# Kernel tuning notes

Hardware: AMD Instinct MI355X
Metric: run time of the kernel (lower is better)

The kernel has to match this reference:

```python
import jax, jax.numpy as jnp
import numpy as np

B, S, D, H = 4, 2048, 768, 12
DH = D // H  # 64
SCALE = float(DH)  # att_scale == 'per_head' -> dim // num_heads


def setup_inputs() -> dict:
    key = jax.random.key(0)
    ks = jax.random.split(key, 7)
    p = 1.0 / np.sqrt(D)
    return {
        "x": jax.random.normal(ks[0], (B, S, D), dtype=jnp.float32),
        "Wq": jax.random.normal(ks[1], (D, D), dtype=jnp.float32) * p,
        "bq": jax.random.normal(ks[2], (D,), dtype=jnp.float32) * p,
        "Wk": jax.random.normal(ks[3], (D, D), dtype=jnp.float32) * p,
        "bk": jax.random.normal(ks[4], (D,), dtype=jnp.float32) * p,
        "Wv": jax.random.normal(ks[5], (D, D), dtype=jnp.float32) * p,
        "bv": jax.random.normal(ks[6], (D,), dtype=jnp.float32) * p,
    }


def reference(x, Wq, bq, Wk, bk, Wv, bv):
    # torch nn.Linear: y = x @ W.T + b
    q = x @ Wq.T + bq  # [B,S,D]
    k = x @ Wk.T + bk
    v = x @ Wv.T + bv
    # split heads -> [B,H,S,DH]
    def heads(t):
        return t.reshape(B, S, H, DH).transpose(0, 2, 1, 3)
    q, k, v = heads(q), heads(k), heads(v)
    scores = jnp.einsum("bhqd,bhkd->bhqk", q, k) / jnp.sqrt(jnp.float32(SCALE))
    probs = jax.nn.softmax(scores, axis=-1)
    h = jnp.einsum("bhqk,bhkd->bhqd", probs, v)  # [B,H,S,DH]
    return h.transpose(0, 2, 1, 3).reshape(B, S, D)
```

## Files before the change

### kernel.cpp

```cpp
#include <hip/hip_runtime.h>

#define NB 4
#define NS 2048
#define ND 768
#define NH 12
#define NDH 64
#define NM (NB * NS)

typedef __attribute__((ext_vector_type(8))) _Float16 f16x8;
typedef __attribute__((ext_vector_type(4))) _Float16 f16x4;
typedef __attribute__((ext_vector_type(2))) _Float16 f16x2;
typedef __attribute__((ext_vector_type(8))) unsigned short u16x8;
typedef __attribute__((ext_vector_type(4))) unsigned short u16x4;
typedef __attribute__((ext_vector_type(4))) float f32x4;

__device__ __forceinline__ unsigned short f2h(float f) {
    _Float16 h = (_Float16)f;
    return __builtin_bit_cast(unsigned short, h);
}
__device__ __forceinline__ f16x8 ldf16x8(const unsigned short* p) {
    return __builtin_bit_cast(f16x8, *(const u16x8*)p);
}
__device__ __forceinline__ f16x4 ldf16x4(const unsigned short* p) {
    return __builtin_bit_cast(f16x4, *(const u16x4*)p);
}
__device__ __forceinline__ void gload_lds16(const void* g, void* l) {
    __builtin_amdgcn_global_load_lds(
        (const __attribute__((address_space(1))) void*)g,
        (__attribute__((address_space(3))) void*)l, 16, 0, 0);
}

__device__ __forceinline__ float exp2_fast(float x) {
#if __has_builtin(__builtin_amdgcn_exp2f)
    return __builtin_amdgcn_exp2f(x);
#else
    return exp2f(x);
#endif
}

__device__ __forceinline__ float max3f(float a, float b, float c) {
    return fmaxf(fmaxf(a, b), c);
}

__device__ __forceinline__ f16x4 pk4(float a, float b, float c, float d) {
#if __has_builtin(__builtin_amdgcn_cvt_pkrtz)
    f16x2 lo = __builtin_bit_cast(f16x2, __builtin_amdgcn_cvt_pkrtz(a, b));
    f16x2 hi = __builtin_bit_cast(f16x2, __builtin_amdgcn_cvt_pkrtz(c, d));
    f16x4 r;
    r[0] = lo[0]; r[1] = lo[1]; r[2] = hi[0]; r[3] = hi[1];
    return r;
#else
    f16x4 r;
    r[0] = (_Float16)a; r[1] = (_Float16)b;
    r[2] = (_Float16)c; r[3] = (_Float16)d;
    return r;
#endif
}

__global__ __launch_bounds__(256)
void conv_f32_to_f16(const float* __restrict__ x,
                     const float* __restrict__ wq,
                     const float* __restrict__ wk,
                     const float* __restrict__ wv,
                     unsigned short* __restrict__ dst)
{
    const int CX = (NM * ND) / 8;
    const int CW = (ND * ND) / 8;
    int c = blockIdx.x * 256 + threadIdx.x;
    const float* src;
    int base;
    if (c < CX)               { src = x;  base = 0; }
    else if (c < CX + CW)     { src = wq; base = CX; }
    else if (c < CX + 2 * CW) { src = wk; base = CX + CW; }
    else                      { src = wv; base = CX + 2 * CW; }
    const float4* p = (const float4*)&src[(size_t)(c - base) * 8];
    float4 a = p[0], b = p[1];
    u16x8 r;
    r[0] = f2h(a.x); r[1] = f2h(a.y); r[2] = f2h(a.z); r[3] = f2h(a.w);
    r[4] = f2h(b.x); r[5] = f2h(b.y); r[6] = f2h(b.z); r[7] = f2h(b.w);
    *(u16x8*)&dst[(size_t)c * 8] = r;
}

__global__ __launch_bounds__(256)
void qkv_gemm(const unsigned short* __restrict__ xh,
              const unsigned short* __restrict__ wh,
              const float* __restrict__ bq,
              const float* __restrict__ bk,
              const float* __restrict__ bv,
              unsigned short* __restrict__ qkv)
{
    const int z = blockIdx.z;
    const unsigned short* W = wh + (size_t)z * ND * ND;
    const float* bias = (z == 0) ? bq : (z == 1) ? bk : bv;
    unsigned short* out = qkv + (size_t)z * NM * ND;

    const int m0 = blockIdx.x * 128;
    const int n0 = blockIdx.y * 128;
    const int tid = threadIdx.x;
    const int lane = tid & 63, wave = tid >> 6;
    const int quad = lane >> 4, l16 = lane & 15;
    const int wm = (wave >> 1) * 64, wn = (wave & 1) * 64;

    __shared__ __align__(16) unsigned short As[128 * 32];
    __shared__ __align__(16) unsigned short Bs[128 * 32];

    const f32x4 fz = {0.f, 0.f, 0.f, 0.f};
    f32x4 acc[4][4];
#pragma unroll
    for (int i = 0; i < 4; ++i)
#pragma unroll
        for (int j = 0; j < 4; ++j) acc[i][j] = fz;

    const int lrow = lane >> 2;
    const int lcol = (lane & 3) * 8;

    for (int kt = 0; kt < ND / 32; ++kt) {
        const int k0 = kt * 32;
        __syncthreads();
#pragma unroll
        for (int i = 0; i < 2; ++i) {
            const int seg = wave * 2 + i;
            const int row = seg * 16 + lrow;
            gload_lds16(&xh[(size_t)(m0 + row) * ND + k0 + lcol], &As[seg * 512]);
            gload_lds16(&W[(size_t)(n0 + row) * ND + k0 + lcol], &Bs[seg * 512]);
        }
        __syncthreads();

        f16x8 af[4], bf_[4];
#pragma unroll
        for (int mi = 0; mi < 4; ++mi)
            af[mi] = ldf16x8(&As[(wm + mi * 16 + l16) * 32 + quad * 8]);
#pragma unroll
        for (int ni = 0; ni < 4; ++ni)
            bf_[ni] = ldf16x8(&Bs[(wn + ni * 16 + l16) * 32 + quad * 8]);
#pragma unroll
        for (int mi = 0; mi < 4; ++mi)
#pragma unroll
            for (int ni = 0; ni < 4; ++ni)
                acc[mi][ni] = __builtin_amdgcn_mfma_f32_16x16x32_f16(
                    af[mi], bf_[ni], acc[mi][ni], 0, 0, 0);
    }

#pragma unroll
    for (int ni = 0; ni < 4; ++ni) {
        const int n = n0 + wn + ni * 16 + l16;
        const float bval = bias[n];
        const int hh = n >> 6, d = n & 63;
#pragma unroll
        for (int mi = 0; mi < 4; ++mi) {
#pragma unroll
            for (int r = 0; r < 4; ++r) {
                const int m = m0 + wm + mi * 16 + quad * 4 + r;
                const int bi = m >> 11, s = m & (NS - 1);
                out[(((size_t)(bi * NH + hh)) * NS + s) * NDH + d] =
                    f2h(acc[mi][ni][r] + bval);
            }
        }
    }
}

#define KLD 132

__global__ __launch_bounds__(256)
void attn_kernel(const unsigned short* __restrict__ qh,
                 const unsigned short* __restrict__ kh,
                 const unsigned short* __restrict__ vh,
                 float* __restrict__ out)
{
    const int bh = blockIdx.y;
    const int bb = bh / NH, hh = bh % NH;
    const int tid = threadIdx.x;
    const int lane = tid & 63, wave = tid >> 6;
    const int quad = lane >> 4, l16 = lane & 15;
    const int q0 = blockIdx.x * 128 + wave * 32;

    __shared__ __align__(16) unsigned short Ks[128 * 64];
    __shared__ __align__(16) unsigned short VTs[64 * KLD];

    const unsigned short* qb = qh + (size_t)bh * NS * NDH;
    const unsigned short* kb = kh + (size_t)bh * NS * NDH;
    const unsigned short* vb = vh + (size_t)bh * NS * NDH;

    f16x8 bq_[2][2];
#pragma unroll
    for (int qt = 0; qt < 2; ++qt)
#pragma unroll
        for (int kk = 0; kk < 2; ++kk)
            bq_[qt][kk] = ldf16x8(
                &qb[(size_t)(q0 + qt * 16 + l16) * NDH + kk * 32 + quad * 8]);

    const float c2 = 0.18033688011112042f;

    const f32x4 fz = {0.f, 0.f, 0.f, 0.f};
    f32x4 o[2][4];
    float m2[2], lsum[2];
#pragma unroll
    for (int qt = 0; qt < 2; ++qt) {
#pragma unroll
        for (int dt = 0; dt < 4; ++dt) o[qt][dt] = fz;
        m2[qt] = -__builtin_inff();
        lsum[qt] = 0.f;
    }

    const int krow = tid >> 3;
    const int kcol = (tid & 7) * 8;
    const int kcolS = 8 * ((tid & 7) ^ (krow & 7));
    const int vpair = tid & 31;
    const int vchunk = tid >> 5;

    const int rdsw = (l16 & 7) << 3;

    const unsigned short* kp = kb + (size_t)krow * NDH + kcol;
    const unsigned short* vp = vb + (size_t)(2 * vpair) * NDH + vchunk * 8;

    u16x8 kr[4], vr0[2], vr1[2];
#pragma unroll
    for (int i = 0; i < 4; ++i)
        kr[i] = *(const u16x8*)(kp + i * (32 * NDH));
#pragma unroll
    for (int i2 = 0; i2 < 2; ++i2) {
        vr0[i2] = *(const u16x8*)(vp + i2 * (64 * NDH));
        vr1[i2] = *(const u16x8*)(vp + i2 * (64 * NDH) + NDH);
    }

    const int NT = NS / 128;
    for (int kt = 0; kt < NT; ++kt) {
        __syncthreads();
#pragma unroll
        for (int i = 0; i < 4; ++i)
            *(u16x8*)&Ks[(krow + i * 32) * 64 + kcolS] = kr[i];
#pragma unroll
        for (int i2 = 0; i2 < 2; ++i2) {
            const int P = vpair + i2 * 32;
#pragma unroll
            for (int j = 0; j < 8; ++j) {
                unsigned pk = (unsigned)vr0[i2][j] | ((unsigned)vr1[i2][j] << 16);
                *(unsigned*)&VTs[(vchunk * 8 + j) * KLD + 2 * P] = pk;
            }
        }
        kp += 128 * NDH;
        vp += 128 * NDH;
        if (kt + 1 < NT) {
#pragma unroll
            for (int i = 0; i < 4; ++i)
                kr[i] = *(const u16x8*)(kp + i * (32 * NDH));
#pragma unroll
            for (int i2 = 0; i2 < 2; ++i2) {
                vr0[i2] = *(const u16x8*)(vp + i2 * (64 * NDH));
                vr1[i2] = *(const u16x8*)(vp + i2 * (64 * NDH) + NDH);
            }
        }
        __syncthreads();

#pragma unroll
        for (int half = 0; half < 2; ++half) {
            const int kvb = half * 64;

            f16x8 ak[4][2];
#pragma unroll
            for (int kvt = 0; kvt < 4; ++kvt)
#pragma unroll
                for (int kk = 0; kk < 2; ++kk)
                    ak[kvt][kk] = ldf16x8(
                        &Ks[(kvb + kvt * 16 + l16) * 64 +
                            ((kk * 32 + quad * 8) ^ rdsw)]);

            f32x4 st[2][4];
            __builtin_amdgcn_s_setprio(1);
#pragma unroll
            for (int qt = 0; qt < 2; ++qt)
#pragma unroll
                for (int kvt = 0; kvt < 4; ++kvt) {
                    st[qt][kvt] = fz;
#pragma unroll
                    for (int kk = 0; kk < 2; ++kk)
                        st[qt][kvt] = __builtin_amdgcn_mfma_f32_16x16x32_f16(
                            ak[kvt][kk], bq_[qt][kk], st[qt][kvt], 0, 0, 0);
                }
            __builtin_amdgcn_s_setprio(0);

            f16x4 av[4][4];
#pragma unroll
            for (int dt = 0; dt < 4; ++dt)
#pragma unroll
                for (int kvt = 0; kvt < 4; ++kvt)
                    av[dt][kvt] = ldf16x4(
                        &VTs[(dt * 16 + l16) * KLD + kvb + kvt * 16 + quad * 4]);

#pragma unroll
            for (int qt = 0; qt < 2; ++qt) {
                const float r0 = max3f(st[qt][0][0], st[qt][0][1], st[qt][0][2]);
                const float r1 = max3f(st[qt][0][3], st[qt][1][0], st[qt][1][1]);
                const float r2 = max3f(st[qt][1][2], st[qt][1][3], st[qt][2][0]);
                const float r3 = max3f(st[qt][2][1], st[qt][2][2], st[qt][2][3]);
                const float r4 = max3f(st[qt][3][0], st[qt][3][1], st[qt][3][2]);
                float rm = fmaxf(max3f(r0, r1, r2), max3f(r3, r4, st[qt][3][3]));

                if (!__all(rm * c2 <= m2[qt] + 8.f)) {
                    rm = fmaxf(rm, __shfl_xor(rm, 16, 64));
                    rm = fmaxf(rm, __shfl_xor(rm, 32, 64));
                    const float mn = fmaxf(m2[qt], rm * c2);
                    const float al = exp2_fast(m2[qt] - mn);
                    m2[qt] = mn;
                    lsum[qt] *= al;
#pragma unroll
                    for (int dt = 0; dt < 4; ++dt)
                        o[qt][dt] *= al;
                }
                const float mn = m2[qt];

                float rs = 0.f;
                f16x4 pf[4];
#pragma unroll
                for (int kvt = 0; kvt < 4; ++kvt) {
                    const float p0 = exp2_fast(fmaf(st[qt][kvt][0], c2, -mn));
                    const float p1 = exp2_fast(fmaf(st[qt][kvt][1], c2, -mn));
                    const float p2 = exp2_fast(fmaf(st[qt][kvt][2], c2, -mn));
                    const float p3 = exp2_fast(fmaf(st[qt][kvt][3], c2, -mn));
                    rs += (p0 + p1) + (p2 + p3);
                    pf[kvt] = pk4(p0, p1, p2, p3);
                }
                lsum[qt] += rs;

                __builtin_amdgcn_s_setprio(1);
#pragma unroll
                for (int dt = 0; dt < 4; ++dt)
#pragma unroll
                    for (int kvt = 0; kvt < 4; ++kvt)
                        o[qt][dt] = __builtin_amdgcn_mfma_f32_16x16x16f16(
                            av[dt][kvt], pf[kvt], o[qt][dt], 0, 0, 0);
                __builtin_amdgcn_s_setprio(0);
            }
        }
    }

#pragma unroll
    for (int qt = 0; qt < 2; ++qt) {
        const int q = q0 + qt * 16 + l16;
        float l = lsum[qt];
        l += __shfl_xor(l, 16, 64);
        l += __shfl_xor(l, 32, 64);
        const float inv = 1.f / l;
#pragma unroll
        for (int dt = 0; dt < 4; ++dt) {
            float4 v;
            v.x = o[qt][dt][0] * inv;
            v.y = o[qt][dt][1] * inv;
            v.z = o[qt][dt][2] * inv;
            v.w = o[qt][dt][3] * inv;
            *(float4*)&out[((size_t)(bb * NS + q)) * ND + hh * NDH + dt * 16 + quad * 4] = v;
        }
    }
}

extern "C" void kernel_launch(void* const* d_in, const int* in_sizes, int n_in,
                              void* d_out, int out_size, void* d_ws, size_t ws_size,
                              hipStream_t stream)
{
    const float* x  = (const float*)d_in[0];
    const float* Wq = (const float*)d_in[1];
    const float* bq = (const float*)d_in[2];
    const float* Wk = (const float*)d_in[3];
    const float* bk = (const float*)d_in[4];
    const float* Wv = (const float*)d_in[5];
    const float* bv = (const float*)d_in[6];

    unsigned short* ws  = (unsigned short*)d_ws;
    unsigned short* xh  = ws;
    unsigned short* wh  = xh + (size_t)NM * ND;
    unsigned short* qkv = wh + (size_t)3 * ND * ND;
    unsigned short* qhp = qkv;
    unsigned short* khp = qkv + (size_t)NM * ND;
    unsigned short* vhp = qkv + (size_t)2 * NM * ND;

    const int convBlocks = (NM * ND + 3 * ND * ND) / (8 * 256);
    conv_f32_to_f16<<<convBlocks, 256, 0, stream>>>(x, Wq, Wk, Wv, xh);

    qkv_gemm<<<dim3(NM / 128, ND / 128, 3), 256, 0, stream>>>(
        xh, wh, bq, bk, bv, qkv);

    attn_kernel<<<dim3(NS / 128, NB * NH), 256, 0, stream>>>(
        qhp, khp, vhp, (float*)d_out);
}
```

Baseline: 215.4 us.

## Widen QKV GEMM K-tile to 64 with XOR-swizzled LDS and grouped block order

The QKV projection GEMM now stages 64-wide K slices instead of 32, which halves the number of barrier pairs per tile. LDS rows use an XOR swizzle on the 16-byte column chunk to avoid bank conflicts on the wider rows. The 3D grid is flattened into a 1D grid with a grouped mapping, so 8 consecutive M tiles sweep all 18 N/z tiles together for better L2 reuse of the x rows. LDS use doubles to 32 KB per block, which may reduce occupancy.

Result: slower. 224.1 us (+4.0%).

```diff
diff --git a/kernel.cpp b/kernel.cpp
--- a/kernel.cpp
+++ b/kernel.cpp
@@ -89,56 +89,68 @@
               const float* __restrict__ bv,
               unsigned short* __restrict__ qkv)
 {
-    const int z = blockIdx.z;
+    const int bid = blockIdx.x;
+    const int r = bid & 7;
+    const int t = bid >> 3;
+    const int gi = t / 18;
+    const int j  = t % 18;
+    const int m0 = (gi * 8 + r) * 128;
+    const int z  = j / 6;
+    const int n0 = (j % 6) * 128;
+
     const unsigned short* W = wh + (size_t)z * ND * ND;
     const float* bias = (z == 0) ? bq : (z == 1) ? bk : bv;
     unsigned short* out = qkv + (size_t)z * NM * ND;
 
-    const int m0 = blockIdx.x * 128;
-    const int n0 = blockIdx.y * 128;
     const int tid = threadIdx.x;
     const int lane = tid & 63, wave = tid >> 6;
     const int quad = lane >> 4, l16 = lane & 15;
     const int wm = (wave >> 1) * 64, wn = (wave & 1) * 64;
 
-    __shared__ __align__(16) unsigned short As[128 * 32];
-    __shared__ __align__(16) unsigned short Bs[128 * 32];
+    __shared__ __align__(16) unsigned short As[128 * 64];
+    __shared__ __align__(16) unsigned short Bs[128 * 64];
 
     const f32x4 fz = {0.f, 0.f, 0.f, 0.f};
     f32x4 acc[4][4];
 #pragma unroll
     for (int i = 0; i < 4; ++i)
 #pragma unroll
-        for (int j = 0; j < 4; ++j) acc[i][j] = fz;
-
-    const int lrow = lane >> 2;
-    const int lcol = (lane & 3) * 8;
-
-    for (int kt = 0; kt < ND / 32; ++kt) {
-        const int k0 = kt * 32;
+        for (int j2 = 0; j2 < 4; ++j2) acc[i][j2] = fz;
+
+    const int lrow8 = lane >> 3;
+    const int swcb  = (lane & 7) ^ lrow8;
+    const int rsw   = l16 & 7;
+
+    for (int kt = 0; kt < ND / 64; ++kt) {
+        const int k0 = kt * 64;
         __syncthreads();
 #pragma unroll
-        for (int i = 0; i < 2; ++i) {
-            const int seg = wave * 2 + i;
-            const int row = seg * 16 + lrow;
-            gload_lds16(&xh[(size_t)(m0 + row) * ND + k0 + lcol], &As[seg * 512]);
-            gload_lds16(&W[(size_t)(n0 + row) * ND + k0 + lcol], &Bs[seg * 512]);
+        for (int i = 0; i < 4; ++i) {
+            const int seg = wave * 4 + i;
+            const int row = seg * 8 + lrow8;
+            gload_lds16(&xh[(size_t)(m0 + row) * ND + k0 + swcb * 8], &As[seg * 512]);
+            gload_lds16(&W[(size_t)(n0 + row) * ND + k0 + swcb * 8], &Bs[seg * 512]);
         }
         __syncthreads();
 
-        f16x8 af[4], bf_[4];
-#pragma unroll
-        for (int mi = 0; mi < 4; ++mi)
-            af[mi] = ldf16x8(&As[(wm + mi * 16 + l16) * 32 + quad * 8]);
-#pragma unroll
-        for (int ni = 0; ni < 4; ++ni)
-            bf_[ni] = ldf16x8(&Bs[(wn + ni * 16 + l16) * 32 + quad * 8]);
-#pragma unroll
-        for (int mi = 0; mi < 4; ++mi)
+#pragma unroll
+        for (int kk = 0; kk < 2; ++kk) {
+            f16x8 af[4], bf_[4];
+#pragma unroll
+            for (int mi = 0; mi < 4; ++mi)
+                af[mi] = ldf16x8(
+                    &As[(wm + mi * 16 + l16) * 64 + (((kk * 4 + quad) ^ rsw) * 8)]);
 #pragma unroll
             for (int ni = 0; ni < 4; ++ni)
-                acc[mi][ni] = __builtin_amdgcn_mfma_f32_16x16x32_f16(
-                    af[mi], bf_[ni], acc[mi][ni], 0, 0, 0);
+                bf_[ni] = ldf16x8(
+                    &Bs[(wn + ni * 16 + l16) * 64 + (((kk * 4 + quad) ^ rsw) * 8)]);
+#pragma unroll
+            for (int mi = 0; mi < 4; ++mi)
+#pragma unroll
+                for (int ni = 0; ni < 4; ++ni)
+                    acc[mi][ni] = __builtin_amdgcn_mfma_f32_16x16x32_f16(
+                        af[mi], bf_[ni], acc[mi][ni], 0, 0, 0);
+        }
     }
 
 #pragma unroll
@@ -149,11 +161,11 @@
 #pragma unroll
         for (int mi = 0; mi < 4; ++mi) {
 #pragma unroll
-            for (int r = 0; r < 4; ++r) {
-                const int m = m0 + wm + mi * 16 + quad * 4 + r;
+            for (int r2 = 0; r2 < 4; ++r2) {
+                const int m = m0 + wm + mi * 16 + quad * 4 + r2;
                 const int bi = m >> 11, s = m & (NS - 1);
                 out[(((size_t)(bi * NH + hh)) * NS + s) * NDH + d] =
-                    f2h(acc[mi][ni][r] + bval);
+                    f2h(acc[mi][ni][r2] + bval);
             }
         }
     }
@@ -376,8 +388,7 @@
     const int convBlocks = (NM * ND + 3 * ND * ND) / (8 * 256);
     conv_f32_to_f16<<<convBlocks, 256, 0, stream>>>(x, Wq, Wk, Wv, xh);
 
-    qkv_gemm<<<dim3(NM / 128, ND / 128, 3), 256, 0, stream>>>(
-        xh, wh, bq, bk, bv, qkv);
+    qkv_gemm<<<dim3(1152), 256, 0, stream>>>(xh, wh, bq, bk, bv, qkv);
 
     attn_kernel<<<dim3(NS / 128, NB * NH), 256, 0, stream>>>(
         qhp, khp, vhp, (float*)d_out);
```

## Rewrite QKV GEMM with 256x256 tiles, double-buffered swizzled LDS and interleaved prefetch

Applied to the files above, without the earlier changes.

The QKV projection GEMM now runs 512-thread blocks on 256x256 output tiles with a K-step of 64, treating the three weight matrices as one 2304-wide N dimension. Shared memory is double-buffered with an XOR-swizzled layout to avoid bank conflicts. Loads for the next K tile are issued in between MFMA groups, with barriers and s_setprio to overlap memory traffic with matrix math. This targets the previous kernel's load-sync-compute serialization and its low data reuse, at the cost of 128KB of LDS per block, higher register pressure and fewer, larger blocks.

Measured after the change: 226.1 us. 5.0% more time.

```diff
diff --git a/kernel.cpp b/kernel.cpp
--- a/kernel.cpp
+++ b/kernel.cpp
@@ -56,6 +56,10 @@
     return r;
 #endif
 }
+
+#define GBAR() do { asm volatile("" ::: "memory");            \
+                    __builtin_amdgcn_s_barrier();             \
+                    asm volatile("" ::: "memory"); } while (0)
 
 __global__ __launch_bounds__(256)
 void conv_f32_to_f16(const float* __restrict__ x,
@@ -81,7 +85,7 @@
     *(u16x8*)&dst[(size_t)c * 8] = r;
 }
 
-__global__ __launch_bounds__(256)
+__global__ __launch_bounds__(512, 2)
 void qkv_gemm(const unsigned short* __restrict__ xh,
               const unsigned short* __restrict__ wh,
               const float* __restrict__ bq,
@@ -89,71 +93,145 @@
               const float* __restrict__ bv,
               unsigned short* __restrict__ qkv)
 {
-    const int z = blockIdx.z;
-    const unsigned short* W = wh + (size_t)z * ND * ND;
-    const float* bias = (z == 0) ? bq : (z == 1) ? bk : bv;
-    unsigned short* out = qkv + (size_t)z * NM * ND;
-
-    const int m0 = blockIdx.x * 128;
-    const int n0 = blockIdx.y * 128;
+    const int m0 = blockIdx.x * 256;
+    const int n0 = blockIdx.y * 256;
+    const int z  = blockIdx.y / 3;
+
     const int tid = threadIdx.x;
     const int lane = tid & 63, wave = tid >> 6;
     const int quad = lane >> 4, l16 = lane & 15;
-    const int wm = (wave >> 1) * 64, wn = (wave & 1) * 64;
-
-    __shared__ __align__(16) unsigned short As[128 * 32];
-    __shared__ __align__(16) unsigned short Bs[128 * 32];
+    const int wave_m = wave >> 2;
+    const int wave_n = wave & 3;
+
+    __shared__ __align__(16) unsigned short LDS[8 * 8192];
 
     const f32x4 fz = {0.f, 0.f, 0.f, 0.f};
-    f32x4 acc[4][4];
-#pragma unroll
-    for (int i = 0; i < 4; ++i)
+    f32x4 acc[8][4];
+#pragma unroll
+    for (int i = 0; i < 8; ++i)
 #pragma unroll
         for (int j = 0; j < 4; ++j) acc[i][j] = fz;
 
-    const int lrow = lane >> 2;
-    const int lcol = (lane & 3) * 8;
-
-    for (int kt = 0; kt < ND / 32; ++kt) {
-        const int k0 = kt * 32;
-        __syncthreads();
-#pragma unroll
-        for (int i = 0; i < 2; ++i) {
-            const int seg = wave * 2 + i;
-            const int row = seg * 16 + lrow;
-            gload_lds16(&xh[(size_t)(m0 + row) * ND + k0 + lcol], &As[seg * 512]);
-            gload_lds16(&W[(size_t)(n0 + row) * ND + k0 + lcol], &Bs[seg * 512]);
-        }
-        __syncthreads();
-
-        f16x8 af[4], bf_[4];
-#pragma unroll
-        for (int mi = 0; mi < 4; ++mi)
-            af[mi] = ldf16x8(&As[(wm + mi * 16 + l16) * 32 + quad * 8]);
-#pragma unroll
-        for (int ni = 0; ni < 4; ++ni)
-            bf_[ni] = ldf16x8(&Bs[(wn + ni * 16 + l16) * 32 + quad * 8]);
-#pragma unroll
-        for (int mi = 0; mi < 4; ++mi)
-#pragma unroll
-            for (int ni = 0; ni < 4; ++ni)
-                acc[mi][ni] = __builtin_amdgcn_mfma_f32_16x16x32_f16(
-                    af[mi], bf_[ni], acc[mi][ni], 0, 0, 0);
-    }
-
-#pragma unroll
-    for (int ni = 0; ni < 4; ++ni) {
-        const int n = n0 + wn + ni * 16 + l16;
-        const float bval = bias[n];
-        const int hh = n >> 6, d = n & 63;
-#pragma unroll
-        for (int mi = 0; mi < 4; ++mi) {
+    const int sA = tid, sB = tid + 512;
+    const int rA = sA >> 3, cbA = (((sA & 7) ^ (rA & 7)) << 3);
+    const int rB = sB >> 3, cbB = (((sB & 7) ^ (rB & 7)) << 3);
+
+    auto stage_half = [&](int kt2, int sub) {
+        const int slot = ((kt2 & 1) * 4 + sub);
+        const int k0 = kt2 * 64;
+        const unsigned short* s0;
+        const unsigned short* s1;
+        if (sub < 2) {
+            s0 = &xh[(size_t)(m0 + sub * 128 + rA) * ND + k0 + cbA];
+            s1 = &xh[(size_t)(m0 + sub * 128 + rB) * ND + k0 + cbB];
+        } else {
+            s0 = &wh[(size_t)(n0 + (sub - 2) * 128 + rA) * ND + k0 + cbA];
+            s1 = &wh[(size_t)(n0 + (sub - 2) * 128 + rB) * ND + k0 + cbB];
+        }
+        gload_lds16(s0, &LDS[(size_t)slot * 8192 + (size_t)sA * 8]);
+        gload_lds16(s1, &LDS[(size_t)slot * 8192 + (size_t)sB * 8]);
+    };
+
+    auto ldfrag = [&](int slot, int r, int g) -> f16x8 {
+        return ldf16x8(&LDS[slot * 8192 + r * 64 + ((g ^ (r & 7)) << 3)]);
+    };
+
+    stage_half(0, 0); stage_half(0, 1); stage_half(0, 2); stage_half(0, 3);
+    asm volatile("s_waitcnt vmcnt(0)" ::: "memory");
+    GBAR();
+
+#define MFMA_QUAD(Q, A0K0, A0K1, A1K0, A1K1)                                  \
+    __builtin_amdgcn_s_setprio(1);                                            \
+    _Pragma("unroll")                                                         \
+    for (int nrep = 0; nrep < 4; ++nrep) {                                    \
+        acc[2*(Q)][nrep] = __builtin_amdgcn_mfma_f32_16x16x32_f16(            \
+            A0K0, bf[nrep][0], acc[2*(Q)][nrep], 0, 0, 0);                    \
+        acc[2*(Q)][nrep] = __builtin_amdgcn_mfma_f32_16x16x32_f16(            \
+            A0K1, bf[nrep][1], acc[2*(Q)][nrep], 0, 0, 0);                    \
+        acc[2*(Q)+1][nrep] = __builtin_amdgcn_mfma_f32_16x16x32_f16(          \
+            A1K0, bf[nrep][0], acc[2*(Q)+1][nrep], 0, 0, 0);                  \
+        acc[2*(Q)+1][nrep] = __builtin_amdgcn_mfma_f32_16x16x32_f16(          \
+            A1K1, bf[nrep][1], acc[2*(Q)+1][nrep], 0, 0, 0);                  \
+    }                                                                         \
+    __builtin_amdgcn_s_setprio(0);
+
+    for (int kt = 0; kt < ND / 64; ++kt) {
+        const int cbuf = (kt & 1) * 4;
+        const bool more = (kt + 1) < ND / 64;
+        const int aslot = cbuf + wave_m;
+
+        if (more) { stage_half(kt + 1, 0); stage_half(kt + 1, 1); }
+        f16x8 bf[4][2];
+#pragma unroll
+        for (int nrep = 0; nrep < 4; ++nrep) {
+            const int nl = wave_n * 64 + nrep * 16 + l16;
+            const int bslot = cbuf + 2 + (nl >> 7);
+            const int br = nl & 127;
+            bf[nrep][0] = ldfrag(bslot, br, quad);
+            bf[nrep][1] = ldfrag(bslot, br, 4 + quad);
+        }
+        {
+            const int r0 = 0 * 16 + l16, r1 = 1 * 16 + l16;
+            f16x8 a00 = ldfrag(aslot, r0, quad);
+            f16x8 a01 = ldfrag(aslot, r0, 4 + quad);
+            f16x8 a10 = ldfrag(aslot, r1, quad);
+            f16x8 a11 = ldfrag(aslot, r1, 4 + quad);
+            GBAR();
+            MFMA_QUAD(0, a00, a01, a10, a11)
+            GBAR();
+        }
+        if (more) stage_half(kt + 1, 2);
+        {
+            const int r0 = 2 * 16 + l16, r1 = 3 * 16 + l16;
+            f16x8 a00 = ldfrag(aslot, r0, quad);
+            f16x8 a01 = ldfrag(aslot, r0, 4 + quad);
+            f16x8 a10 = ldfrag(aslot, r1, quad);
+            f16x8 a11 = ldfrag(aslot, r1, 4 + quad);
+            GBAR();
+            MFMA_QUAD(1, a00, a01, a10, a11)
+            GBAR();
+        }
+        if (more) stage_half(kt + 1, 3);
+        {
+            const int r0 = 4 * 16 + l16, r1 = 5 * 16 + l16;
+            f16x8 a00 = ldfrag(aslot, r0, quad);
+            f16x8 a01 = ldfrag(aslot, r0, 4 + quad);
+            f16x8 a10 = ldfrag(aslot, r1, quad);
+            f16x8 a11 = ldfrag(aslot, r1, 4 + quad);
+            GBAR();
+            MFMA_QUAD(2, a00, a01, a10, a11)
+            GBAR();
+        }
+        {
+            const int r0 = 6 * 16 + l16, r1 = 7 * 16 + l16;
+            f16x8 a00 = ldfrag(aslot, r0, quad);
+            f16x8 a01 = ldfrag(aslot, r0, 4 + quad);
+            f16x8 a10 = ldfrag(aslot, r1, quad);
+            f16x8 a11 = ldfrag(aslot, r1, 4 + quad);
+            GBAR();
+            MFMA_QUAD(3, a00, a01, a10, a11)
+            asm volatile("s_waitcnt vmcnt(0)" ::: "memory");
+            GBAR();
+        }
+    }
+#undef MFMA_QUAD
+
+    const float* bias = (z == 0) ? bq : (z == 1) ? bk : bv;
+    unsigned short* outz = qkv + (size_t)z * NM * ND;
+    const int nbase = n0 - z * ND + wave_n * 64;
+#pragma unroll
+    for (int nrep = 0; nrep < 4; ++nrep) {
+        const int nl = nbase + nrep * 16 + l16;
+        const float bval = bias[nl];
+        const int hh = nl >> 6, d = nl & 63;
+#pragma unroll
+        for (int mrep = 0; mrep < 8; ++mrep) {
 #pragma unroll
             for (int r = 0; r < 4; ++r) {
-                const int m = m0 + wm + mi * 16 + quad * 4 + r;
+                const int m = m0 + wave_m * 128 + mrep * 16 + quad * 4 + r;
                 const int bi = m >> 11, s = m & (NS - 1);
-                out[(((size_t)(bi * NH + hh)) * NS + s) * NDH + d] =
-                    f2h(acc[mi][ni][r] + bval);
+                outz[(((size_t)(bi * NH + hh)) * NS + s) * NDH + d] =
+                    f2h(acc[mrep][nrep][r] + bval);
             }
         }
     }
@@ -376,7 +454,7 @@
     const int convBlocks = (NM * ND + 3 * ND * ND) / (8 * 256);
     conv_f32_to_f16<<<convBlocks, 256, 0, stream>>>(x, Wq, Wk, Wv, xh);
 
-    qkv_gemm<<<dim3(NM / 128, ND / 128, 3), 256, 0, stream>>>(
+    qkv_gemm<<<dim3(NM / 256, (3 * ND) / 256), 512, 0, stream>>>(
         xh, wh, bq, bk, bv, qkv);
 
     attn_kernel<<<dim3(NS / 128, NB * NH), 256, 0, stream>>>(
```

## Halve attention query tile per block and swizzle transposed V in LDS

Applied to the files above, without the earlier changes.

Each wave now processes 16 query rows instead of 32, so each block covers 64 queries and the grid doubles. This cuts per-thread registers and adds more blocks for latency hiding, but every block must reload and restage the full K/V stream, doubling K/V global and LDS traffic. The padded V-transpose layout is replaced by an XOR-swizzled layout to avoid bank conflicts without padding.

After: 237.9 us. 10.5% more time.

```diff
diff --git a/kernel.cpp b/kernel.cpp
--- a/kernel.cpp
+++ b/kernel.cpp
@@ -159,8 +159,6 @@
     }
 }
 
-#define KLD 132
-
 __global__ __launch_bounds__(256)
 void attn_kernel(const unsigned short* __restrict__ qh,
                  const unsigned short* __restrict__ kh,
@@ -172,35 +170,27 @@
     const int tid = threadIdx.x;
     const int lane = tid & 63, wave = tid >> 6;
     const int quad = lane >> 4, l16 = lane & 15;
-    const int q0 = blockIdx.x * 128 + wave * 32;
+    const int q0 = blockIdx.x * 64 + wave * 16;
 
     __shared__ __align__(16) unsigned short Ks[128 * 64];
-    __shared__ __align__(16) unsigned short VTs[64 * KLD];
+    __shared__ __align__(16) unsigned short VTs[64 * 128];
 
     const unsigned short* qb = qh + (size_t)bh * NS * NDH;
     const unsigned short* kb = kh + (size_t)bh * NS * NDH;
     const unsigned short* vb = vh + (size_t)bh * NS * NDH;
 
-    f16x8 bq_[2][2];
-#pragma unroll
-    for (int qt = 0; qt < 2; ++qt)
-#pragma unroll
-        for (int kk = 0; kk < 2; ++kk)
-            bq_[qt][kk] = ldf16x8(
-                &qb[(size_t)(q0 + qt * 16 + l16) * NDH + kk * 32 + quad * 8]);
+    f16x8 bq_[2];
+#pragma unroll
+    for (int kk = 0; kk < 2; ++kk)
+        bq_[kk] = ldf16x8(&qb[(size_t)(q0 + l16) * NDH + kk * 32 + quad * 8]);
 
     const float c2 = 0.18033688011112042f;
 
     const f32x4 fz = {0.f, 0.f, 0.f, 0.f};
-    f32x4 o[2][4];
-    float m2[2], lsum[2];
-#pragma unroll
-    for (int qt = 0; qt < 2; ++qt) {
-#pragma unroll
-        for (int dt = 0; dt < 4; ++dt) o[qt][dt] = fz;
-        m2[qt] = -__builtin_inff();
-        lsum[qt] = 0.f;
-    }
+    f32x4 o[4];
+    float m2 = -__builtin_inff(), lsum = 0.f;
+#pragma unroll
+    for (int dt = 0; dt < 4; ++dt) o[dt] = fz;
 
     const int krow = tid >> 3;
     const int kcol = (tid & 7) * 8;
@@ -234,8 +224,9 @@
             const int P = vpair + i2 * 32;
 #pragma unroll
             for (int j = 0; j < 8; ++j) {
+                const int row = vchunk * 8 + j;
                 unsigned pk = (unsigned)vr0[i2][j] | ((unsigned)vr1[i2][j] << 16);
-                *(unsigned*)&VTs[(vchunk * 8 + j) * KLD + 2 * P] = pk;
+                *(unsigned*)&VTs[row * 128 + ((2 * P) ^ ((row & 7) << 3))] = pk;
             }
         }
         kp += 128 * NDH;
@@ -265,18 +256,16 @@
                         &Ks[(kvb + kvt * 16 + l16) * 64 +
                             ((kk * 32 + quad * 8) ^ rdsw)]);
 
-            f32x4 st[2][4];
+            f32x4 st[4];
             __builtin_amdgcn_s_setprio(1);
 #pragma unroll
-            for (int qt = 0; qt < 2; ++qt)
-#pragma unroll
-                for (int kvt = 0; kvt < 4; ++kvt) {
-                    st[qt][kvt] = fz;
-#pragma unroll
-                    for (int kk = 0; kk < 2; ++kk)
-                        st[qt][kvt] = __builtin_amdgcn_mfma_f32_16x16x32_f16(
-                            ak[kvt][kk], bq_[qt][kk], st[qt][kvt], 0, 0, 0);
-                }
+            for (int kvt = 0; kvt < 4; ++kvt) {
+                st[kvt] = fz;
+#pragma unroll
+                for (int kk = 0; kk < 2; ++kk)
+                    st[kvt] = __builtin_amdgcn_mfma_f32_16x16x32_f16(
+                        ak[kvt][kk], bq_[kk], st[kvt], 0, 0, 0);
+            }
             __builtin_amdgcn_s_setprio(0);
 
             f16x4 av[4][4];
@@ -285,69 +274,68 @@
 #pragma unroll
                 for (int kvt = 0; kvt < 4; ++kvt)
                     av[dt][kvt] = ldf16x4(
-                        &VTs[(dt * 16 + l16) * KLD + kvb + kvt * 16 + quad * 4]);
-
-#pragma unroll
-            for (int qt = 0; qt < 2; ++qt) {
-                const float r0 = max3f(st[qt][0][0], st[qt][0][1], st[qt][0][2]);
-                const float r1 = max3f(st[qt][0][3], st[qt][1][0], st[qt][1][1]);
-                const float r2 = max3f(st[qt][1][2], st[qt][1][3], st[qt][2][0]);
-                const float r3 = max3f(st[qt][2][1], st[qt][2][2], st[qt][2][3]);
-                const float r4 = max3f(st[qt][3][0], st[qt][3][1], st[qt][3][2]);
-                float rm = fmaxf(max3f(r0, r1, r2), max3f(r3, r4, st[qt][3][3]));
-
-                if (!__all(rm * c2 <= m2[qt] + 8.f)) {
+                        &VTs[(dt * 16 + l16) * 128 +
+                             ((kvb + kvt * 16 + quad * 4) ^ rdsw)]);
+
+            {
+                const float r0 = max3f(st[0][0], st[0][1], st[0][2]);
+                const float r1 = max3f(st[0][3], st[1][0], st[1][1]);
+                const float r2 = max3f(st[1][2], st[1][3], st[2][0]);
+                const float r3 = max3f(st[2][1], st[2][2], st[2][3]);
+                const float r4 = max3f(st[3][0], st[3][1], st[3][2]);
+                float rm = fmaxf(max3f(r0, r1, r2), max3f(r3, r4, st[3][3]));
+
+                if (!__all(rm * c2 <= m2 + 8.f)) {
                     rm = fmaxf(rm, __shfl_xor(rm, 16, 64));
                     rm = fmaxf(rm, __shfl_xor(rm, 32, 64));
-                    const float mn = fmaxf(m2[qt], rm * c2);
-                    const float al = exp2_fast(m2[qt] - mn);
-                    m2[qt] = mn;
-                    lsum[qt] *= al;
+                    const float mn = fmaxf(m2, rm * c2);
+                    const float al = exp2_fast(m2 - mn);
+                    m2 = mn;
+                    lsum *= al;
 #pragma unroll
                     for (int dt = 0; dt < 4; ++dt)
-                        o[qt][dt] *= al;
+                        o[dt] *= al;
                 }
-                const float mn = m2[qt];
+                const float mn = m2;
 
                 float rs = 0.f;
                 f16x4 pf[4];
 #pragma unroll
                 for (int kvt = 0; kvt < 4; ++kvt) {
-                    const float p0 = exp2_fast(fmaf(st[qt][kvt][0], c2, -mn));
-                    const float p1 = exp2_fast(fmaf(st[qt][kvt][1], c2, -mn));
-                    const float p2 = exp2_fast(fmaf(st[qt][kvt][2], c2, -mn));
-                    const float p3 = exp2_fast(fmaf(st[qt][kvt][3], c2, -mn));
+                    const float p0 = exp2_fast(fmaf(st[kvt][0], c2, -mn));
+                    const float p1 = exp2_fast(fmaf(st[kvt][1], c2, -mn));
+                    const float p2 = exp2_fast(fmaf(st[kvt][2], c2, -mn));
+                    const float p3 = exp2_fast(fmaf(st[kvt][3], c2, -mn));
                     rs += (p0 + p1) + (p2 + p3);
                     pf[kvt] = pk4(p0, p1, p2, p3);
                 }
-                lsum[qt] += rs;
+                lsum += rs;
 
                 __builtin_amdgcn_s_setprio(1);
 #pragma unroll
                 for (int dt = 0; dt < 4; ++dt)
 #pragma unroll
                     for (int kvt = 0; kvt < 4; ++kvt)
-                        o[qt][dt] = __builtin_amdgcn_mfma_f32_16x16x16f16(
-                            av[dt][kvt], pf[kvt], o[qt][dt], 0, 0, 0);
+                        o[dt] = __builtin_amdgcn_mfma_f32_16x16x16f16(
+                            av[dt][kvt], pf[kvt], o[dt], 0, 0, 0);
                 __builtin_amdgcn_s_setprio(0);
             }
         }
     }
 
-#pragma unroll
-    for (int qt = 0; qt < 2; ++qt) {
-        const int q = q0 + qt * 16 + l16;
-        float l = lsum[qt];
+    {
+        const int q = q0 + l16;
+        float l = lsum;
         l += __shfl_xor(l, 16, 64);
         l += __shfl_xor(l, 32, 64);
         const float inv = 1.f / l;
 #pragma unroll
         for (int dt = 0; dt < 4; ++dt) {
             float4 v;
-            v.x = o[qt][dt][0] * inv;
-            v.y = o[qt][dt][1] * inv;
-            v.z = o[qt][dt][2] * inv;
-            v.w = o[qt][dt][3] * inv;
+            v.x = o[dt][0] * inv;
+            v.y = o[dt][1] * inv;
+            v.z = o[dt][2] * inv;
+            v.w = o[dt][3] * inv;
             *(float4*)&out[((size_t)(bb * NS + q)) * ND + hh * NDH + dt * 16 + quad * 4] = v;
         }
     }
@@ -379,6 +367,6 @@
     qkv_gemm<<<dim3(NM / 128, ND / 128, 3), 256, 0, stream>>>(
         xh, wh, bq, bk, bv, qkv);
 
-    attn_kernel<<<dim3(NS / 128, NB * NH), 256, 0, stream>>>(
+    attn_kernel<<<dim3(NS / 64, NB * NH), 256, 0, stream>>>(
         qhp, khp, vhp, (float*)d_out);
 }
```
